# Performance work log

Measured on AMD Instinct MI355X. Metric: run time of the kernel, lower is better.

## Reference

```python
import jax, jax.numpy as jnp
import numpy as np

EMBED_DIM = 768
N_HEADS = 12
TIME_RATIO = 0.5
HEAD_DIM = EMBED_DIM // N_HEADS          # 64
T_HEAD = int(HEAD_DIM * TIME_RATIO)      # 32 time dims per head
T_DIM = T_HEAD * N_HEADS                 # 384 time dims overall
EPS = 1e-5


def _ln(v, g, b):
    m = jnp.mean(v, axis=-1, keepdims=True)
    var = jnp.mean((v - m) ** 2, axis=-1, keepdims=True)
    return (v - m) * jax.lax.rsqrt(var + EPS) * g + b


def minkowski_ln(x, g_t, b_t, g_s, b_s):
    # normalize time-like and space-like channel groups separately
    xt, xs = x[..., :T_DIM], x[..., T_DIM:]
    return jnp.concatenate([_ln(xt, g_t, b_t), _ln(xs, g_s, b_s)], axis=-1)


def lorentz_attention(x, Wq, bq, Wk, bk, Wv, bv, Wo, bo):
    B, S, D = x.shape
    def heads(W, b):
        return (x @ W + b).reshape(B, S, N_HEADS, HEAD_DIM).transpose(0, 2, 1, 3)
    q, k, v = heads(Wq, bq), heads(Wk, bk), heads(Wv, bv)
    # Minkowski metric signature (-,...,-,+,...,+) within each head
    eta = jnp.concatenate([-jnp.ones((T_HEAD,), x.dtype), jnp.ones((HEAD_DIM - T_HEAD,), x.dtype)])
    logits = jnp.einsum('bhqd,bhkd->bhqk', q * eta, k) / np.sqrt(HEAD_DIM).astype(np.float32)
    attn = jax.nn.softmax(logits, axis=-1)
    o = jnp.einsum('bhqk,bhkd->bhqd', attn, v)
    o = o.transpose(0, 2, 1, 3).reshape(B, S, D)
    return o @ Wo + bo


def setup_inputs() -> dict:
    key = jax.random.key(0)
    ks = jax.random.split(key, 16)
    D, H4 = EMBED_DIM, EMBED_DIM * 4
    s = 0.02
    inp = {
        'x': jax.random.normal(ks[0], (2, 2048, D), jnp.float32),
        'Wq': jax.random.normal(ks[1], (D, D), jnp.float32) * s, 'bq': jnp.zeros((D,), jnp.float32),
        'Wk': jax.random.normal(ks[2], (D, D), jnp.float32) * s, 'bk': jnp.zeros((D,), jnp.float32),
        'Wv': jax.random.normal(ks[3], (D, D), jnp.float32) * s, 'bv': jnp.zeros((D,), jnp.float32),
        'Wo': jax.random.normal(ks[4], (D, D), jnp.float32) * s, 'bo': jnp.zeros((D,), jnp.float32),
        'g1t': jnp.ones((T_DIM,), jnp.float32), 'b1t': jnp.zeros((T_DIM,), jnp.float32),
        'g1s': jnp.ones((D - T_DIM,), jnp.float32), 'b1s': jnp.zeros((D - T_DIM,), jnp.float32),
        'W1': jax.random.normal(ks[5], (D, H4), jnp.float32) * s, 'bb1': jnp.zeros((H4,), jnp.float32),
        'W2': jax.random.normal(ks[6], (H4, D), jnp.float32) * s, 'bb2': jnp.zeros((D,), jnp.float32),
        'g2t': jnp.ones((T_DIM,), jnp.float32), 'b2t': jnp.zeros((T_DIM,), jnp.float32),
        'g2s': jnp.ones((D - T_DIM,), jnp.float32), 'b2s': jnp.zeros((D - T_DIM,), jnp.float32),
    }
    return inp


def reference(x, Wq, bq, Wk, bk, Wv, bv, Wo, bo,
              g1t, b1t, g1s, b1s, W1, bb1, W2, bb2,
              g2t, b2t, g2s, b2s):
    a = lorentz_attention(x, Wq, bq, Wk, bk, Wv, bv, Wo, bo)
    x = minkowski_ln(x + a, g1t, b1t, g1s, b1s)
    h = jax.nn.gelu(x @ W1 + bb1) @ W2 + bb2
    x = minkowski_ln(x + h, g2t, b2t, g2s, b2s)
    return x
```

## Files before the change

### kernel.cpp

```cpp
#include <hip/hip_runtime.h>
#include <cstddef>
#include <cstdint>

#define D_EMB  768
#define NHEAD  12
#define HDIM   64
#define THEAD  32
#define SEQ    2048
#define BATCH  2
#define NROW   (BATCH*SEQ)
#define HID4   3072

typedef unsigned short u16;
typedef __bf16 bf16x8 __attribute__((ext_vector_type(8)));
typedef float  f32x4  __attribute__((ext_vector_type(4)));
typedef unsigned short u16x8 __attribute__((ext_vector_type(8)));

__device__ __forceinline__ u16 f2bf(float f) {
    unsigned u = __builtin_bit_cast(unsigned, f);
    return (u16)((u + 0x7FFFu + ((u >> 16) & 1u)) >> 16);
}

__device__ __forceinline__ void gload_lds16(const void* g, void* l) {
    __builtin_amdgcn_global_load_lds(
        reinterpret_cast<const __attribute__((address_space(1))) void*>(
            reinterpret_cast<uintptr_t>(g)),
        reinterpret_cast<__attribute__((address_space(3))) void*>(
            (uint32_t)reinterpret_cast<uintptr_t>(l)),
        16, 0, 0);
}

__device__ __forceinline__ void tcast(float (*t)[33], const float* __restrict__ W,
                                      u16* __restrict__ WT, int K, int M,
                                      int mt, int kt)
{
    const int m0 = mt * 32, k0 = kt * 32;
    const int tx = threadIdx.x & 31, ty = threadIdx.x >> 5;
#pragma unroll
    for (int i = 0; i < 32; i += 8)
        t[ty + i][tx] = W[(size_t)(k0 + ty + i) * M + m0 + tx];
    __syncthreads();
#pragma unroll
    for (int i = 0; i < 32; i += 8)
        WT[(size_t)(m0 + ty + i) * K + k0 + tx] = f2bf(t[tx][ty + i]);
}

__global__ __launch_bounds__(256)
void prep(const float* __restrict__ Wq, const float* __restrict__ Wk,
          const float* __restrict__ Wv, const float* __restrict__ Wo,
          const float* __restrict__ W1, const float* __restrict__ W2,
          const float* __restrict__ bq, const float* __restrict__ bk,
          const float* __restrict__ bv, const float* __restrict__ x,
          u16* __restrict__ WqkvoT, u16* __restrict__ W1T,
          u16* __restrict__ W2T, u16* __restrict__ xb,
          float* __restrict__ bqkv)
{
    __shared__ float t[32][33];
    const int bid = blockIdx.x;
    if (bid < 2304) {
        const int z = bid / 576, r = bid % 576;
        const float* W = z == 0 ? Wq : z == 1 ? Wk : z == 2 ? Wv : Wo;
        tcast(t, W, WqkvoT + (size_t)z * 768 * 768, 768, 768, r % 24, r / 24);
    } else if (bid < 4608) {
        const int r = bid - 2304;
        tcast(t, W1, W1T, 768, 3072, r % 96, r / 96);
    } else if (bid < 6912) {
        const int r = bid - 4608;
        tcast(t, W2, W2T, 3072, 768, r % 24, r / 24);
    } else if (bid < 8448) {
        const int i = (bid - 6912) * 2048 + threadIdx.x * 8;
        const float4 a = *reinterpret_cast<const float4*>(x + i);
        const float4 b = *reinterpret_cast<const float4*>(x + i + 4);
        u16x8 h;
        h[0] = f2bf(a.x); h[1] = f2bf(a.y); h[2] = f2bf(a.z); h[3] = f2bf(a.w);
        h[4] = f2bf(b.x); h[5] = f2bf(b.y); h[6] = f2bf(b.z); h[7] = f2bf(b.w);
        *reinterpret_cast<u16x8*>(xb + i) = h;
    } else {
        const int i = (bid - 8448) * 256 + threadIdx.x;
        if (i < 2304)
            bqkv[i] = i < 768 ? bq[i] : (i < 1536 ? bk[i - 768] : bv[i - 1536]);
    }
}

template<int EPI>
__global__ __launch_bounds__(256)
void gemm_bf16(const u16* __restrict__ A, const u16* __restrict__ B,
               const float* __restrict__ bias, void* __restrict__ Cp,
               u16* __restrict__ VTp, int K, int N)
{
    __shared__ u16 As[2][128 * 32];
    __shared__ u16 Bs[2][128 * 32];
    const int tid  = threadIdx.x;
    const int lane = tid & 63;
    const int w    = tid >> 6;
    const int m0 = blockIdx.x * 128, n0 = blockIdx.y * 128;
    const int wr = (w >> 1) << 6, wc = (w & 1) << 6;

    const int seg0 = (w << 11) + lane * 16;
    const int row0 = seg0 >> 6, cb0 = (seg0 & 63) >> 1;
    const int seg1 = seg0 + 1024;
    const int row1 = seg1 >> 6, cb1 = (seg1 & 63) >> 1;
    const u16* a0 = A + (size_t)(m0 + row0) * K + cb0;
    const u16* a1 = A + (size_t)(m0 + row1) * K + cb1;
    const u16* b0 = B + (size_t)(n0 + row0) * K + cb0;
    const u16* b1 = B + (size_t)(n0 + row1) * K + cb1;
    const int lo0 = (w * 2 + 0) << 9;
    const int lo1 = (w * 2 + 1) << 9;

    int aIdx[4], bIdx[4];
#pragma unroll
    for (int i = 0; i < 4; ++i) {
        aIdx[i] = (wr + i * 16 + (lane & 15)) * 32 + ((lane >> 4) << 3);
        bIdx[i] = (wc + i * 16 + (lane & 15)) * 32 + ((lane >> 4) << 3);
    }

    f32x4 acc[4][4];
#pragma unroll
    for (int i = 0; i < 4; ++i)
#pragma unroll
        for (int j = 0; j < 4; ++j)
#pragma unroll
            for (int q = 0; q < 4; ++q) acc[i][j][q] = 0.f;

    gload_lds16(a0, &As[0][lo0]);
    gload_lds16(a1, &As[0][lo1]);
    gload_lds16(b0, &Bs[0][lo0]);
    gload_lds16(b1, &Bs[0][lo1]);
    __syncthreads();

    int cur = 0;
    for (int k0 = 0; k0 < K; k0 += 32) {
        if (k0 + 32 < K) {
            gload_lds16(a0 + k0 + 32, &As[cur ^ 1][lo0]);
            gload_lds16(a1 + k0 + 32, &As[cur ^ 1][lo1]);
            gload_lds16(b0 + k0 + 32, &Bs[cur ^ 1][lo0]);
            gload_lds16(b1 + k0 + 32, &Bs[cur ^ 1][lo1]);
        }
        bf16x8 af[4], bv[4];
#pragma unroll
        for (int i = 0; i < 4; ++i)
            af[i] = *reinterpret_cast<const bf16x8*>(&As[cur][aIdx[i]]);
#pragma unroll
        for (int j = 0; j < 4; ++j)
            bv[j] = *reinterpret_cast<const bf16x8*>(&Bs[cur][bIdx[j]]);
#pragma unroll
        for (int i = 0; i < 4; ++i)
#pragma unroll
            for (int j = 0; j < 4; ++j)
                acc[i][j] = __builtin_amdgcn_mfma_f32_16x16x32_bf16(
                    af[i], bv[j], acc[i][j], 0, 0, 0);
        __syncthreads();
        cur ^= 1;
    }

#pragma unroll
    for (int i = 0; i < 4; ++i) {
#pragma unroll
        for (int q = 0; q < 4; ++q) {
            const int row = m0 + wr + i * 16 + ((lane >> 4) << 2) + q;
#pragma unroll
            for (int j = 0; j < 4; ++j) {
                const int col = n0 + wc + j * 16 + (lane & 15);
                float v = acc[i][j][q] + bias[col];
                if (EPI == 2) {
                    const float u3 = v * v * v;
                    v = 0.5f * v * (1.f + tanhf(0.7978845608028654f *
                                                (v + 0.044715f * u3)));
                    ((u16*)Cp)[(size_t)row * N + col] = f2bf(v);
                } else {
                    if (n0 < 1536) {
                        ((u16*)Cp)[(size_t)row * 1536 + col] = f2bf(v);
                    } else {
                        const int c2 = col - 1536;
                        const int hh = c2 >> 6, dd = c2 & 63;
                        const int bb = row >> 11, tok = row & 2047;
                        const int t = tok & 63;
                        const int p = ((t & 15) << 2) | (t >> 4);
                        VTp[((size_t)(bb * NHEAD + hh) * HDIM + dd) * SEQ
                            + (tok & ~63) + p] = f2bf(v);
                    }
                }
            }
        }
    }
}

__global__ __launch_bounds__(256)
void gemm_n64(const u16* __restrict__ A, const u16* __restrict__ B,
              const float* __restrict__ bias, float* __restrict__ C,
              int K, int N)
{
    __shared__ u16 As[2][64 * 32];
    __shared__ u16 Bs[2][128 * 32];
    const int tid  = threadIdx.x;
    const int lane = tid & 63;
    const int w    = tid >> 6;
    const int l15  = lane & 15;
    const int g    = lane >> 4;
    const int m0 = blockIdx.x * 64, n0 = blockIdx.y * 128;

    const int segA = (w << 10) + lane * 16;
    const int rowA = segA >> 6, cbA = (segA & 63) >> 1;
    const u16* aP = A + (size_t)(m0 + rowA) * K + cbA;
    const int loA = w << 9;
    const int seg0 = (w << 11) + lane * 16;
    const int row0 = seg0 >> 6, cb0 = (seg0 & 63) >> 1;
    const int seg1 = seg0 + 1024;
    const int row1 = seg1 >> 6, cb1 = (seg1 & 63) >> 1;
    const u16* b0 = B + (size_t)(n0 + row0) * K + cb0;
    const u16* b1 = B + (size_t)(n0 + row1) * K + cb1;
    const int lo0 = w << 10, lo1 = (w << 10) + 512;

    int aIdx[4], bIdx[2];
#pragma unroll
    for (int i = 0; i < 4; ++i) aIdx[i] = (i * 16 + l15) * 32 + (g << 3);
#pragma unroll
    for (int j = 0; j < 2; ++j) bIdx[j] = ((w << 5) + j * 16 + l15) * 32 + (g << 3);

    f32x4 acc[4][2];
#pragma unroll
    for (int i = 0; i < 4; ++i)
#pragma unroll
        for (int j = 0; j < 2; ++j)
#pragma unroll
            for (int q = 0; q < 4; ++q) acc[i][j][q] = 0.f;

    gload_lds16(aP, &As[0][loA]);
    gload_lds16(b0, &Bs[0][lo0]);
    gload_lds16(b1, &Bs[0][lo1]);
    __syncthreads();

    int cur = 0;
    for (int k0 = 0; k0 < K; k0 += 32) {
        if (k0 + 32 < K) {
            gload_lds16(aP + k0 + 32, &As[cur ^ 1][loA]);
            gload_lds16(b0 + k0 + 32, &Bs[cur ^ 1][lo0]);
            gload_lds16(b1 + k0 + 32, &Bs[cur ^ 1][lo1]);
        }
        bf16x8 af[4], bv[2];
#pragma unroll
        for (int i = 0; i < 4; ++i)
            af[i] = *reinterpret_cast<const bf16x8*>(&As[cur][aIdx[i]]);
#pragma unroll
        for (int j = 0; j < 2; ++j)
            bv[j] = *reinterpret_cast<const bf16x8*>(&Bs[cur][bIdx[j]]);
#pragma unroll
        for (int i = 0; i < 4; ++i)
#pragma unroll
            for (int j = 0; j < 2; ++j)
                acc[i][j] = __builtin_amdgcn_mfma_f32_16x16x32_bf16(
                    af[i], bv[j], acc[i][j], 0, 0, 0);
        __syncthreads();
        cur ^= 1;
    }

#pragma unroll
    for (int i = 0; i < 4; ++i) {
#pragma unroll
        for (int q = 0; q < 4; ++q) {
            const int row = m0 + i * 16 + (g << 2) + q;
#pragma unroll
            for (int j = 0; j < 2; ++j) {
                const int col = n0 + (w << 5) + j * 16 + l15;
                C[(size_t)row * N + col] = acc[i][j][q] + bias[col];
            }
        }
    }
}

__global__ __launch_bounds__(128)
void attn_mfma(const u16* __restrict__ QK, const u16* __restrict__ VT,
               u16* __restrict__ O)
{
    __shared__ u16 Ks[2][64 * 64];
    __shared__ u16 Vs[2][64 * 64];
    __shared__ u16 Ps[64 * 72];

    const int tid  = threadIdx.x;
    const int lane = tid & 63;
    const int w    = tid >> 6;
    const int l15  = lane & 15;
    const int g    = lane >> 4;
    const int bh   = blockIdx.x;
    const int b    = bh / NHEAD, h = bh % NHEAD;
    const int q0   = blockIdx.y * 64;
    const int bS   = b * SEQ;

    bf16x8 aq[2][2];
#pragma unroll
    for (int qb = 0; qb < 2; ++qb) {
        const u16* Qg = QK + (size_t)(bS + q0 + w * 32 + qb * 16 + l15) * 1536
                        + h * HDIM;
#pragma unroll
        for (int kk = 0; kk < 2; ++kk) {
            u16x8 hq = *reinterpret_cast<const u16x8*>(Qg + kk * 32 + g * 8);
            if (kk == 0) {
#pragma unroll
                for (int j = 0; j < 8; ++j) hq[j] ^= 0x8000u;
            }
            aq[qb][kk] = __builtin_bit_cast(bf16x8, hq);
        }
    }

    const int rl = lane >> 3;
    const int cs = ((lane & 7) ^ rl) << 3;
    const u16* pK = QK + (size_t)(bS + w * 32 + rl) * 1536 + 768 + h * HDIM + cs;
    const u16* pV = VT + ((size_t)(b * NHEAD + h) * HDIM + w * 32 + rl) * SEQ + cs;

    int swz[2];
#pragma unroll
    for (int kk = 0; kk < 2; ++kk)
        swz[kk] = ((kk * 4 + g) ^ (l15 & 7)) << 3;

    f32x4 accO[2][4];
#pragma unroll
    for (int qb = 0; qb < 2; ++qb)
#pragma unroll
        for (int n = 0; n < 4; ++n)
#pragma unroll
            for (int q = 0; q < 4; ++q) accO[qb][n][q] = 0.f;
    float psum[2][4] = {};

#define ATTN_STAGE(c, kt)                                                    \
    do {                                                                     \
        u16* dK = &Ks[c][w * 2048];                                          \
        u16* dV = &Vs[c][w * 2048];                                          \
        _Pragma("unroll")                                                    \
        for (int i = 0; i < 4; ++i) {                                        \
            gload_lds16(pK + (size_t)((kt) + 8 * i) * 1536, dK + 512 * i);   \
            gload_lds16(pV + (size_t)(8 * i) * SEQ + (kt),  dV + 512 * i);   \
        }                                                                    \
    } while (0)

    ATTN_STAGE(0, 0);
    __syncthreads();
    int cur = 0;

    for (int kt = 0; kt < SEQ; kt += 64) {
        if (kt + 64 < SEQ) ATTN_STAGE(cur ^ 1, kt + 64);

        bf16x8 bk[4][2];
#pragma unroll
        for (int n = 0; n < 4; ++n)
#pragma unroll
            for (int kk = 0; kk < 2; ++kk)
                bk[n][kk] = *reinterpret_cast<const bf16x8*>(
                    &Ks[cur][(n * 16 + l15) * 64 + swz[kk]]);

        f32x4 sac[2][4];
#pragma unroll
        for (int qb = 0; qb < 2; ++qb)
#pragma unroll
            for (int n = 0; n < 4; ++n) {
#pragma unroll
                for (int q = 0; q < 4; ++q) sac[qb][n][q] = 0.f;
#pragma unroll
                for (int kk = 0; kk < 2; ++kk)
                    sac[qb][n] = __builtin_amdgcn_mfma_f32_16x16x32_bf16(
                        aq[qb][kk], bk[n][kk], sac[qb][n], 0, 0, 0);
            }

#pragma unroll
        for (int qb = 0; qb < 2; ++qb)
#pragma unroll
            for (int r4 = 0; r4 < 4; ++r4) {
                const int prow = w * 32 + qb * 16 + g * 4 + r4;
                ushort4 pk4;
                float sv0 = __builtin_amdgcn_exp2f(sac[qb][0][r4] * 0.18033688011112042f);
                float sv1 = __builtin_amdgcn_exp2f(sac[qb][1][r4] * 0.18033688011112042f);
                float sv2 = __builtin_amdgcn_exp2f(sac[qb][2][r4] * 0.18033688011112042f);
                float sv3 = __builtin_amdgcn_exp2f(sac[qb][3][r4] * 0.18033688011112042f);
                psum[qb][r4] += sv0 + sv1 + sv2 + sv3;
                pk4.x = f2bf(sv0); pk4.y = f2bf(sv1);
                pk4.z = f2bf(sv2); pk4.w = f2bf(sv3);
                *reinterpret_cast<ushort4*>(&Ps[prow * 72 + (l15 << 2)]) = pk4;
            }

        bf16x8 bv[4][2];
#pragma unroll
        for (int n = 0; n < 4; ++n)
#pragma unroll
            for (int kk = 0; kk < 2; ++kk)
                bv[n][kk] = *reinterpret_cast<const bf16x8*>(
                    &Vs[cur][(n * 16 + l15) * 64 + swz[kk]]);
#pragma unroll
        for (int qb = 0; qb < 2; ++qb) {
            bf16x8 pa[2];
#pragma unroll
            for (int kk = 0; kk < 2; ++kk)
                pa[kk] = *reinterpret_cast<const bf16x8*>(
                    &Ps[(w * 32 + qb * 16 + l15) * 72 + kk * 32 + g * 8]);
#pragma unroll
            for (int n = 0; n < 4; ++n)
#pragma unroll
                for (int kk = 0; kk < 2; ++kk)
                    accO[qb][n] = __builtin_amdgcn_mfma_f32_16x16x32_bf16(
                        pa[kk], bv[n][kk], accO[qb][n], 0, 0, 0);
        }
        __syncthreads();
        cur ^= 1;
    }

#pragma unroll
    for (int qb = 0; qb < 2; ++qb)
#pragma unroll
        for (int r4 = 0; r4 < 4; ++r4) {
            float ps = psum[qb][r4];
#pragma unroll
            for (int off = 1; off < 16; off <<= 1)
                ps += __shfl_xor(ps, off, 16);
            const float inv = 1.f / ps;
            const int qr = q0 + w * 32 + qb * 16 + g * 4 + r4;
#pragma unroll
            for (int n = 0; n < 4; ++n)
                O[(size_t)(bS + qr) * D_EMB + h * HDIM + n * 16 + l15]
                    = f2bf(accO[qb][n][r4] * inv);
        }
#undef ATTN_STAGE
}

__global__ __launch_bounds__(256)
void mink_ln(const float* __restrict__ X, const float* __restrict__ R,
             const float* __restrict__ gt, const float* __restrict__ bt,
             const float* __restrict__ gs, const float* __restrict__ bs,
             float* __restrict__ Out, u16* __restrict__ OutB, int nrows)
{
    const int wid  = (int)((blockIdx.x * 256 + threadIdx.x) >> 6);
    const int lane = threadIdx.x & 63;
    const int row  = wid >> 1, half = wid & 1;
    if (row >= nrows) return;

    const float* g  = half ? gs : gt;
    const float* bb = half ? bs : bt;
    const size_t base = (size_t)row * D_EMB + half * 384;

    float v[6];
    float sum = 0.f;
#pragma unroll
    for (int i = 0; i < 6; ++i) {
        const float t = X[base + i * 64 + lane] + R[base + i * 64 + lane];
        v[i] = t; sum += t;
    }
#pragma unroll
    for (int off = 32; off; off >>= 1) sum += __shfl_xor(sum, off);
    const float mean = sum * (1.f / 384.f);

    float ss = 0.f;
#pragma unroll
    for (int i = 0; i < 6; ++i) { const float d = v[i] - mean; ss += d * d; }
#pragma unroll
    for (int off = 32; off; off >>= 1) ss += __shfl_xor(ss, off);
    const float rstd = rsqrtf(ss * (1.f / 384.f) + 1e-5f);

#pragma unroll
    for (int i = 0; i < 6; ++i) {
        const int e = i * 64 + lane;
        const float o = (v[i] - mean) * rstd * g[e] + bb[e];
        Out[base + e] = o;
        if (OutB) OutB[base + e] = f2bf(o);
    }
}

extern "C" void kernel_launch(void* const* d_in, const int* in_sizes, int n_in,
                              void* d_out, int out_size, void* d_ws, size_t ws_size,
                              hipStream_t stream)
{
    const float* x   = (const float*)d_in[0];
    const float* Wq  = (const float*)d_in[1];
    const float* bq  = (const float*)d_in[2];
    const float* Wk  = (const float*)d_in[3];
    const float* bk  = (const float*)d_in[4];
    const float* Wv  = (const float*)d_in[5];
    const float* bv  = (const float*)d_in[6];
    const float* Wo  = (const float*)d_in[7];
    const float* bo  = (const float*)d_in[8];
    const float* g1t = (const float*)d_in[9];
    const float* b1t = (const float*)d_in[10];
    const float* g1s = (const float*)d_in[11];
    const float* b1s = (const float*)d_in[12];
    const float* W1  = (const float*)d_in[13];
    const float* bb1 = (const float*)d_in[14];
    const float* W2  = (const float*)d_in[15];
    const float* bb2 = (const float*)d_in[16];
    const float* g2t = (const float*)d_in[17];
    const float* b2t = (const float*)d_in[18];
    const float* g2s = (const float*)d_in[19];
    const float* b2s = (const float*)d_in[20];
    float* out = (float*)d_out;

    const size_t ND = (size_t)NROW * D_EMB;
    u16* WqkvoT = (u16*)d_ws;
    u16* W1T = WqkvoT + 2359296;
    u16* W2T = W1T + 2359296;
    u16* xb  = W2T + 2359296;
    u16* QKb = xb + ND;
    u16* VTb = QKb + (size_t)NROW * 1536;
    u16* Ab  = VTb + ND;
    u16* Hb  = QKb;
    float* AoF  = (float*)(Ab + ND);
    float* bqkv = AoF;
    float* X1   = AoF + ND;

    const dim3 blk(256);

    prep<<<8457, blk, 0, stream>>>(Wq, Wk, Wv, Wo, W1, W2, bq, bk, bv, x,
                                   WqkvoT, W1T, W2T, xb, bqkv);

    gemm_bf16<3><<<dim3(32, 18), blk, 0, stream>>>(xb, WqkvoT, bqkv, QKb, VTb,
                                                   768, 2304);
    attn_mfma<<<dim3(BATCH * NHEAD, SEQ / 64), dim3(128), 0, stream>>>(QKb, VTb, Ab);

    gemm_n64<<<dim3(64, 6), blk, 0, stream>>>(Ab, WqkvoT + (size_t)2304 * 768,
                                              bo, AoF, 768, 768);
    mink_ln<<<2048, blk, 0, stream>>>(x, AoF, g1t, b1t, g1s, b1s, X1, xb, NROW);
    gemm_bf16<2><<<dim3(32, 24), blk, 0, stream>>>(xb, W1T, bb1, Hb, nullptr,
                                                   768, 3072);
    gemm_n64<<<dim3(64, 6), blk, 0, stream>>>(Hb, W2T, bb2, AoF, 3072, 768);
    mink_ln<<<2048, blk, 0, stream>>>(X1, AoF, g2t, b2t, g2s, b2s, out, nullptr, NROW);
}
```

Measured before the change: 209.0 us.

## Split attention across four waves, fold scale into Q, use MFMA row sums

The attention kernel now runs 256 threads (four waves), each wave owning 16 query rows instead of 32, so every wave issues half the MFMAs and K/V tile loading is spread over more waves. The softmax scale and Minkowski sign are folded into Q once up front, which removes a multiply per score. The row-sum is now computed with an extra MFMA against a ones vector using the bf16-rounded probabilities, replacing the VALU accumulation and the final shuffle reduction. In exchange there are more waves per block, higher LDS read traffic per MFMA, and Q is rounded to bf16 after scaling.

```diff
diff --git a/kernel.cpp b/kernel.cpp
--- a/kernel.cpp
+++ b/kernel.cpp
@@ -19,6 +19,9 @@
 __device__ __forceinline__ u16 f2bf(float f) {
     unsigned u = __builtin_bit_cast(unsigned, f);
     return (u16)((u + 0x7FFFu + ((u >> 16) & 1u)) >> 16);
+}
+__device__ __forceinline__ float bf2f(u16 h) {
+    return __builtin_bit_cast(float, (unsigned)h << 16);
 }
 
 __device__ __forceinline__ void gload_lds16(const void* g, void* l) {
@@ -268,7 +271,9 @@
     }
 }
 
-__global__ __launch_bounds__(128)
+#define SM_SCALE 0.18033688011112042f
+
+__global__ __launch_bounds__(256)
 void attn_mfma(const u16* __restrict__ QK, const u16* __restrict__ VT,
                u16* __restrict__ O)
 {
@@ -286,50 +291,56 @@
     const int q0   = blockIdx.y * 64;
     const int bS   = b * SEQ;
 
-    bf16x8 aq[2][2];
-#pragma unroll
-    for (int qb = 0; qb < 2; ++qb) {
-        const u16* Qg = QK + (size_t)(bS + q0 + w * 32 + qb * 16 + l15) * 1536
-                        + h * HDIM;
+    bf16x8 aq[2];
+    {
+        const u16* Qg = QK + (size_t)(bS + q0 + (w << 4) + l15) * 1536 + h * HDIM;
 #pragma unroll
         for (int kk = 0; kk < 2; ++kk) {
-            u16x8 hq = *reinterpret_cast<const u16x8*>(Qg + kk * 32 + g * 8);
-            if (kk == 0) {
-#pragma unroll
-                for (int j = 0; j < 8; ++j) hq[j] ^= 0x8000u;
-            }
-            aq[qb][kk] = __builtin_bit_cast(bf16x8, hq);
+            const u16x8 hq = *reinterpret_cast<const u16x8*>(Qg + kk * 32 + g * 8);
+            const float sc = (kk == 0) ? -SM_SCALE : SM_SCALE;
+            u16x8 hs;
+#pragma unroll
+            for (int j = 0; j < 8; ++j)
+                hs[j] = __builtin_bit_cast(u16, (__bf16)(bf2f(hq[j]) * sc));
+            aq[kk] = __builtin_bit_cast(bf16x8, hs);
         }
     }
 
     const int rl = lane >> 3;
     const int cs = ((lane & 7) ^ rl) << 3;
-    const u16* pK = QK + (size_t)(bS + w * 32 + rl) * 1536 + 768 + h * HDIM + cs;
-    const u16* pV = VT + ((size_t)(b * NHEAD + h) * HDIM + w * 32 + rl) * SEQ + cs;
+    const u16* pK = QK + (size_t)(bS + 16 * w + rl) * 1536 + 768 + h * HDIM + cs;
+    const u16* pV = VT + ((size_t)(b * NHEAD + h) * HDIM + 16 * w + rl) * SEQ + cs;
 
     int swz[2];
 #pragma unroll
     for (int kk = 0; kk < 2; ++kk)
         swz[kk] = ((kk * 4 + g) ^ (l15 & 7)) << 3;
 
-    f32x4 accO[2][4];
-#pragma unroll
-    for (int qb = 0; qb < 2; ++qb)
-#pragma unroll
-        for (int n = 0; n < 4; ++n)
-#pragma unroll
-            for (int q = 0; q < 4; ++q) accO[qb][n][q] = 0.f;
-    float psum[2][4] = {};
-
-#define ATTN_STAGE(c, kt)                                                    \
-    do {                                                                     \
-        u16* dK = &Ks[c][w * 2048];                                          \
-        u16* dV = &Vs[c][w * 2048];                                          \
-        _Pragma("unroll")                                                    \
-        for (int i = 0; i < 4; ++i) {                                        \
-            gload_lds16(pK + (size_t)((kt) + 8 * i) * 1536, dK + 512 * i);   \
-            gload_lds16(pV + (size_t)(8 * i) * SEQ + (kt),  dV + 512 * i);   \
-        }                                                                    \
+    bf16x8 vones;
+    {
+        u16x8 o16;
+#pragma unroll
+        for (int j = 0; j < 8; ++j) o16[j] = 0x3F80u;
+        vones = __builtin_bit_cast(bf16x8, o16);
+    }
+
+    f32x4 accO[4];
+#pragma unroll
+    for (int n = 0; n < 4; ++n)
+#pragma unroll
+        for (int q = 0; q < 4; ++q) accO[n][q] = 0.f;
+    f32x4 accS;
+#pragma unroll
+    for (int q = 0; q < 4; ++q) accS[q] = 0.f;
+
+#define ATTN_STAGE(c, kt)                                                   \
+    do {                                                                    \
+        u16* dK = &Ks[c][w * 1024];                                         \
+        u16* dV = &Vs[c][w * 1024];                                         \
+        gload_lds16(pK + (size_t)(kt) * 1536,       dK);                    \
+        gload_lds16(pK + (size_t)((kt) + 8) * 1536, dK + 512);              \
+        gload_lds16(pV + (kt),           dV);                               \
+        gload_lds16(pV + (kt) + 8 * SEQ, dV + 512);                         \
     } while (0)
 
     ATTN_STAGE(0, 0);
@@ -339,83 +350,67 @@
     for (int kt = 0; kt < SEQ; kt += 64) {
         if (kt + 64 < SEQ) ATTN_STAGE(cur ^ 1, kt + 64);
 
-        bf16x8 bk[4][2];
-#pragma unroll
-        for (int n = 0; n < 4; ++n)
-#pragma unroll
-            for (int kk = 0; kk < 2; ++kk)
-                bk[n][kk] = *reinterpret_cast<const bf16x8*>(
+        f32x4 sac[4];
+#pragma unroll
+        for (int n = 0; n < 4; ++n) {
+#pragma unroll
+            for (int q = 0; q < 4; ++q) sac[n][q] = 0.f;
+#pragma unroll
+            for (int kk = 0; kk < 2; ++kk) {
+                const bf16x8 bk = *reinterpret_cast<const bf16x8*>(
                     &Ks[cur][(n * 16 + l15) * 64 + swz[kk]]);
-
-        f32x4 sac[2][4];
-#pragma unroll
-        for (int qb = 0; qb < 2; ++qb)
-#pragma unroll
-            for (int n = 0; n < 4; ++n) {
-#pragma unroll
-                for (int q = 0; q < 4; ++q) sac[qb][n][q] = 0.f;
-#pragma unroll
-                for (int kk = 0; kk < 2; ++kk)
-                    sac[qb][n] = __builtin_amdgcn_mfma_f32_16x16x32_bf16(
-                        aq[qb][kk], bk[n][kk], sac[qb][n], 0, 0, 0);
+                sac[n] = __builtin_amdgcn_mfma_f32_16x16x32_bf16(
+                    aq[kk], bk, sac[n], 0, 0, 0);
             }
-
-#pragma unroll
-        for (int qb = 0; qb < 2; ++qb)
-#pragma unroll
-            for (int r4 = 0; r4 < 4; ++r4) {
-                const int prow = w * 32 + qb * 16 + g * 4 + r4;
-                ushort4 pk4;
-                float sv0 = __builtin_amdgcn_exp2f(sac[qb][0][r4] * 0.18033688011112042f);
-                float sv1 = __builtin_amdgcn_exp2f(sac[qb][1][r4] * 0.18033688011112042f);
-                float sv2 = __builtin_amdgcn_exp2f(sac[qb][2][r4] * 0.18033688011112042f);
-                float sv3 = __builtin_amdgcn_exp2f(sac[qb][3][r4] * 0.18033688011112042f);
-                psum[qb][r4] += sv0 + sv1 + sv2 + sv3;
-                pk4.x = f2bf(sv0); pk4.y = f2bf(sv1);
-                pk4.z = f2bf(sv2); pk4.w = f2bf(sv3);
-                *reinterpret_cast<ushort4*>(&Ps[prow * 72 + (l15 << 2)]) = pk4;
+        }
+
+#pragma unroll
+        for (int r4 = 0; r4 < 4; ++r4) {
+            const int prow = (w << 4) + (g << 2) + r4;
+            const float sv0 = __builtin_amdgcn_exp2f(sac[0][r4]);
+            const float sv1 = __builtin_amdgcn_exp2f(sac[1][r4]);
+            const float sv2 = __builtin_amdgcn_exp2f(sac[2][r4]);
+            const float sv3 = __builtin_amdgcn_exp2f(sac[3][r4]);
+            ushort4 pk4;
+            pk4.x = __builtin_bit_cast(u16, (__bf16)sv0);
+            pk4.y = __builtin_bit_cast(u16, (__bf16)sv1);
+            pk4.z = __builtin_bit_cast(u16, (__bf16)sv2);
+            pk4.w = __builtin_bit_cast(u16, (__bf16)sv3);
+            *reinterpret_cast<ushort4*>(&Ps[prow * 72 + (l15 << 2)]) = pk4;
+        }
+
+        bf16x8 pa[2];
+#pragma unroll
+        for (int kk = 0; kk < 2; ++kk)
+            pa[kk] = *reinterpret_cast<const bf16x8*>(
+                &Ps[((w << 4) + l15) * 72 + kk * 32 + g * 8]);
+#pragma unroll
+        for (int n = 0; n < 4; ++n) {
+#pragma unroll
+            for (int kk = 0; kk < 2; ++kk) {
+                const bf16x8 bv = *reinterpret_cast<const bf16x8*>(
+                    &Vs[cur][(n * 16 + l15) * 64 + swz[kk]]);
+                accO[n] = __builtin_amdgcn_mfma_f32_16x16x32_bf16(
+                    pa[kk], bv, accO[n], 0, 0, 0);
             }
-
-        bf16x8 bv[4][2];
-#pragma unroll
-        for (int n = 0; n < 4; ++n)
-#pragma unroll
-            for (int kk = 0; kk < 2; ++kk)
-                bv[n][kk] = *reinterpret_cast<const bf16x8*>(
-                    &Vs[cur][(n * 16 + l15) * 64 + swz[kk]]);
-#pragma unroll
-        for (int qb = 0; qb < 2; ++qb) {
-            bf16x8 pa[2];
-#pragma unroll
-            for (int kk = 0; kk < 2; ++kk)
-                pa[kk] = *reinterpret_cast<const bf16x8*>(
-                    &Ps[(w * 32 + qb * 16 + l15) * 72 + kk * 32 + g * 8]);
-#pragma unroll
-            for (int n = 0; n < 4; ++n)
-#pragma unroll
-                for (int kk = 0; kk < 2; ++kk)
-                    accO[qb][n] = __builtin_amdgcn_mfma_f32_16x16x32_bf16(
-                        pa[kk], bv[n][kk], accO[qb][n], 0, 0, 0);
-        }
+        }
+#pragma unroll
+        for (int kk = 0; kk < 2; ++kk)
+            accS = __builtin_amdgcn_mfma_f32_16x16x32_bf16(
+                pa[kk], vones, accS, 0, 0, 0);
         __syncthreads();
         cur ^= 1;
     }
 
 #pragma unroll
-    for (int qb = 0; qb < 2; ++qb)
-#pragma unroll
-        for (int r4 = 0; r4 < 4; ++r4) {
-            float ps = psum[qb][r4];
-#pragma unroll
-            for (int off = 1; off < 16; off <<= 1)
-                ps += __shfl_xor(ps, off, 16);
-            const float inv = 1.f / ps;
-            const int qr = q0 + w * 32 + qb * 16 + g * 4 + r4;
-#pragma unroll
-            for (int n = 0; n < 4; ++n)
-                O[(size_t)(bS + qr) * D_EMB + h * HDIM + n * 16 + l15]
-                    = f2bf(accO[qb][n][r4] * inv);
-        }
+    for (int r4 = 0; r4 < 4; ++r4) {
+        const float inv = 1.f / accS[r4];
+        const int qr = q0 + (w << 4) + (g << 2) + r4;
+#pragma unroll
+        for (int n = 0; n < 4; ++n)
+            O[(size_t)(bS + qr) * D_EMB + h * HDIM + n * 16 + l15]
+                = f2bf(accO[n][r4] * inv);
+    }
 #undef ATTN_STAGE
 }
 
@@ -508,7 +503,7 @@
 
     gemm_bf16<3><<<dim3(32, 18), blk, 0, stream>>>(xb, WqkvoT, bqkv, QKb, VTb,
                                                    768, 2304);
-    attn_mfma<<<dim3(BATCH * NHEAD, SEQ / 64), dim3(128), 0, stream>>>(QKb, VTb, Ab);
+    attn_mfma<<<dim3(BATCH * NHEAD, SEQ / 64), blk, 0, stream>>>(QKb, VTb, Ab);
 
     gemm_n64<<<dim3(64, 6), blk, 0, stream>>>(Ab, WqkvoT + (size_t)2304 * 768,
                                               bo, AoF, 768, 768);
```

New measurement: 195.1 us. -6.6%, faster.
